# Kernel optimization log

Hardware: AMD Instinct MI355X
Metric: run time of the kernel (lower is better)

The kernel has to match this reference:

```python
import jax, jax.numpy as jnp
import numpy as np

B, C, H, W = 4, 256, 64, 64
CH = C // 2  # inner channels


def setup_inputs() -> dict:
    key = jax.random.key(0)
    ks = jax.random.split(key, 9)
    s = 1.0 / np.sqrt(C)
    so = 1.0 / np.sqrt(CH)
    return {
        "x": jax.random.normal(ks[0], (B, C, H, W), dtype=jnp.float32),
        "teta_w": jax.random.uniform(ks[1], (CH, C), jnp.float32, -s, s),
        "teta_b": jax.random.uniform(ks[2], (CH,), jnp.float32, -s, s),
        "fi_w": jax.random.uniform(ks[3], (CH, C), jnp.float32, -s, s),
        "fi_b": jax.random.uniform(ks[4], (CH,), jnp.float32, -s, s),
        "gi_w": jax.random.uniform(ks[5], (CH, C), jnp.float32, -s, s),
        "gi_b": jax.random.uniform(ks[6], (CH,), jnp.float32, -s, s),
        "out_w": jax.random.uniform(ks[7], (C, CH), jnp.float32, -so, so),
        "out_b": jax.random.uniform(ks[8], (C,), jnp.float32, -so, so),
    }


def _conv1x1(x, w, b):
    # x: (B, Cin, H, W), w: (Cout, Cin) -> (B, Cout, H, W)
    return jnp.einsum('bchw,oc->bohw', x, w) + b[None, :, None, None]


def reference(x, teta_w, teta_b, fi_w, fi_b, gi_w, gi_b, out_w, out_b):
    b, c, h, w = x.shape
    n = h * w
    ch = teta_w.shape[0]
    # NOTE: original uses .view (reshape), NOT transpose, to get (B, N, Ch)
    x1 = _conv1x1(x, teta_w, teta_b).reshape(b, ch, n).reshape(b, n, ch)
    x2 = _conv1x1(x, fi_w, fi_b).reshape(b, ch, n)            # (B, Ch, N)
    x3 = _conv1x1(x, gi_w, gi_b).reshape(b, ch, n).reshape(b, n, ch)
    # softmax over dim=1 (rows), as in the original
    attn = jax.nn.softmax(jnp.matmul(x1, x2), axis=1)          # (B, N, N)
    y = jnp.matmul(attn, x3)                                   # (B, N, Ch)
    y = jnp.swapaxes(y, 1, 2).reshape(b, ch, h, w)
    return x + _conv1x1(y, out_w, out_b)
```

## Files before the change

kernel.cpp:

```cpp
#include <hip/hip_runtime.h>
#include <hip/hip_bf16.h>

#define BB 4
#define CC 256
#define CHH 128
#define NN 4096
#define KSHIFT 12.0f

typedef __attribute__((ext_vector_type(8))) short bf16x8;
typedef __attribute__((ext_vector_type(4))) float f32x4;

__device__ __forceinline__ float to_f(float v) { return v; }
__device__ __forceinline__ float to_f(__hip_bfloat16 v) { return __bfloat162float(v); }
__device__ __forceinline__ void st_f(float* p, float v) { *p = v; }
__device__ __forceinline__ void st_f(__hip_bfloat16* p, float v) { *p = __float2bfloat16(v); }
__device__ __forceinline__ unsigned short f2bf(float f) {
    __hip_bfloat16 h = __float2bfloat16(f);
    unsigned short u;
    __builtin_memcpy(&u, &h, 2);
    return u;
}
__device__ __forceinline__ bf16x8 ldb8(const unsigned short* p) { return *(const bf16x8*)p; }

__device__ __forceinline__ void gload_lds16(const unsigned short* g, unsigned short* l) {
    __builtin_amdgcn_global_load_lds(
        (const __attribute__((address_space(1))) unsigned int*)g,
        (__attribute__((address_space(3))) unsigned int*)l, 16, 0, 0);
}

__global__ void detect_kernel(const void* __restrict__ tb, int* __restrict__ flag) {
    if (threadIdx.x == 0) {
        const __hip_bfloat16* p = (const __hip_bfloat16*)tb;
        int big = 0, zeros = 0;
        for (int i = 0; i < 128; ++i) {
            float v = __bfloat162float(p[i]);
            if (!(fabsf(v) <= 0.5f)) big = 1;
            if ((i & 1) == 0 && v == 0.0f) zeros++;
        }
        *flag = (big || zeros >= 32) ? 1 : 0;
    }
}

template <typename T>
__device__ __forceinline__ void prep_body(const T* tw, const T* fw, const T* gw, const T* ow,
                                          const T* tb2, const T* fb, const T* gb, const T* ob,
                                          unsigned short* Wb, unsigned short* OWb,
                                          float* Bf, float* OBf) {
    int idx = blockIdx.x * 256 + threadIdx.x;
    if (idx < 98304) {
        int cv = idx >> 15, rem = idx & 32767;
        const T* src = cv == 0 ? tw : (cv == 1 ? fw : gw);
        Wb[idx] = f2bf(to_f(src[rem]));
    } else if (idx < 131072) {
        OWb[idx - 98304] = f2bf(to_f(ow[idx - 98304]));
    } else if (idx < 131456) {
        int r = idx - 131072;
        int cv = r >> 7, j = r & 127;
        const T* src = cv == 0 ? tb2 : (cv == 1 ? fb : gb);
        Bf[r] = to_f(src[j]);
    } else if (idx < 131712) {
        OBf[idx - 131456] = to_f(ob[idx - 131456]);
    }
}

__global__ void prep_kernel(const void* tw, const void* fw, const void* gw, const void* ow,
                            const void* tb2, const void* fb, const void* gb, const void* ob,
                            const int* __restrict__ flag,
                            unsigned short* Wb, unsigned short* OWb, float* Bf, float* OBf) {
    if (*flag)
        prep_body<float>((const float*)tw, (const float*)fw, (const float*)gw, (const float*)ow,
                         (const float*)tb2, (const float*)fb, (const float*)gb, (const float*)ob,
                         Wb, OWb, Bf, OBf);
    else
        prep_body<__hip_bfloat16>((const __hip_bfloat16*)tw, (const __hip_bfloat16*)fw,
                                  (const __hip_bfloat16*)gw, (const __hip_bfloat16*)ow,
                                  (const __hip_bfloat16*)tb2, (const __hip_bfloat16*)fb,
                                  (const __hip_bfloat16*)gb, (const __hip_bfloat16*)ob,
                                  Wb, OWb, Bf, OBf);
}

template <typename T>
__device__ __forceinline__ void xtrans_body(const T* __restrict__ x, unsigned short* __restrict__ xt) {
    int b = blockIdx.z;
    const T* in = x + (size_t)b * CC * NN;
    unsigned short* out = xt + (size_t)b * NN * CC;
    int p0 = blockIdx.x * 64, c0 = blockIdx.y * 64;
    __shared__ unsigned short t[64][68];
    int flat = threadIdx.x;
#pragma unroll
    for (int tt = 0; tt < 16; ++tt) {
        int id = flat + tt * 256;
        int rr = id >> 6, cc = id & 63;
        t[cc][rr] = f2bf(to_f(in[(size_t)(c0 + rr) * NN + p0 + cc]));
    }
    __syncthreads();
#pragma unroll
    for (int tt = 0; tt < 16; ++tt) {
        int id = flat + tt * 256;
        int pp = id >> 6, jj = id & 63;
        out[(size_t)(p0 + pp) * CC + c0 + jj] = t[pp][jj];
    }
}

__launch_bounds__(256)
__global__ void xtrans_kernel(const void* x, const int* __restrict__ flag,
                              unsigned short* __restrict__ xt) {
    if (*flag) xtrans_body<float>((const float*)x, xt);
    else       xtrans_body<__hip_bfloat16>((const __hip_bfloat16*)x, xt);
}

__launch_bounds__(256)
__global__ void conv3_mfma_kernel(const unsigned short* __restrict__ xt,
                                  const unsigned short* __restrict__ Wb,
                                  const float* __restrict__ Bf,
                                  unsigned short* __restrict__ T1b,
                                  unsigned short* __restrict__ T2t,
                                  unsigned short* __restrict__ T3b) {
    int b = blockIdx.y;
    int p0 = blockIdx.x * 16;
    int flat = threadIdx.x;
    int w = flat >> 6, lane = flat & 63, m = lane & 15, quad = lane >> 4;
    const unsigned short* xrow = xt + ((size_t)b * NN + p0 + m) * CC;
    bf16x8 xf[8];
#pragma unroll
    for (int kc = 0; kc < 8; ++kc)
        xf[kc] = ldb8(&xrow[kc * 32 + quad * 8]);
    unsigned short* t1  = T1b + (size_t)b * CHH * NN;
    unsigned short* t2t = T2t + (size_t)b * CHH * NN;
    unsigned short* t3  = T3b + (size_t)b * CHH * NN;
#pragma unroll
    for (int q = 0; q < 6; ++q) {
        int t = w * 6 + q;
        int cv = t >> 3, ot = t & 7;
        int o0 = ot * 16;
        const unsigned short* wrow = Wb + ((size_t)cv * CHH + o0 + m) * CC;
        f32x4 acc = {0.f, 0.f, 0.f, 0.f};
#pragma unroll
        for (int kc = 0; kc < 8; ++kc) {
            bf16x8 wf = ldb8(&wrow[kc * 32 + quad * 8]);
            acc = __builtin_amdgcn_mfma_f32_16x16x32_bf16(wf, xf[kc], acc, 0, 0, 0);
        }
        unsigned short hv[4];
#pragma unroll
        for (int r = 0; r < 4; ++r)
            hv[r] = f2bf(acc[r] + Bf[cv * CHH + o0 + quad * 4 + r]);
        if (cv == 1) {
            unsigned int lo = (unsigned int)hv[0] | ((unsigned int)hv[1] << 16);
            unsigned int hi = (unsigned int)hv[2] | ((unsigned int)hv[3] << 16);
            int src = (lane & 3) * 16 + (lane >> 2);
            unsigned int tlo = (unsigned int)__shfl((int)lo, src, 64);
            unsigned int thi = (unsigned int)__shfl((int)hi, src, 64);
            unsigned int* dst = (unsigned int*)&t2t[(size_t)(p0 + (lane >> 2)) * CHH +
                                                    o0 + (lane & 3) * 4];
            dst[0] = tlo;
            dst[1] = thi;
        } else {
            unsigned short* outp = (cv == 0) ? t1 : t3;
#pragma unroll
            for (int r = 0; r < 4; ++r)
                outp[(size_t)(o0 + quad * 4 + r) * NN + p0 + m] = hv[r];
        }
    }
}

__launch_bounds__(256)
__global__ void transpose_kernel(const unsigned short* __restrict__ in,
                                 unsigned short* __restrict__ out, int R, int C) {
    int bz = blockIdx.z;
    in  += (size_t)bz * R * C;
    out += (size_t)bz * R * C;
    int c0 = blockIdx.x * 64, r0 = blockIdx.y * 64;
    __shared__ unsigned short t[64][68];
    int flat = threadIdx.x;
#pragma unroll
    for (int tt = 0; tt < 16; ++tt) {
        int id = flat + tt * 256;
        int r = id >> 6, c = id & 63;
        t[c][r] = in[(size_t)(r0 + r) * C + c0 + c];
    }
    __syncthreads();
#pragma unroll
    for (int tt = 0; tt < 16; ++tt) {
        int id = flat + tt * 256;
        int c = id >> 6, r = id & 63;
        out[(size_t)(c0 + c) * R + r0 + r] = t[c][r];
    }
}

__launch_bounds__(256)
__global__ void stats_mfma_kernel(const unsigned short* __restrict__ T1b,
                                  const unsigned short* __restrict__ T2t,
                                  float* __restrict__ Lpart) {
    int blk = blockIdx.x;
    int b = (blk & 7) >> 1;
    int rest = (blk >> 3) * 2 + (blk & 1);
    int strip = rest >> 3, iq = rest & 7;
    int ibase = iq * 512;
    int flat = threadIdx.x;
    int w = flat >> 6, lane = flat & 63, m = lane & 15, quad = lane >> 4;
    const unsigned short* A  = T1b + (size_t)b * CHH * NN;
    const unsigned short* Bt = T2t + (size_t)b * CHH * NN;
    __shared__ unsigned short th[64 * 128];

    int u0w = strip * 128 + w * 32;
    bf16x8 bfr[2][4];
#pragma unroll
    for (int g = 0; g < 2; ++g)
#pragma unroll
        for (int kc = 0; kc < 4; ++kc)
            bfr[g][kc] = ldb8(&Bt[(size_t)(u0w + g * 16 + m) * CHH + kc * 32 + quad * 8]);

    float csum[2] = {0.f, 0.f};
    for (int t = 0; t < 8; ++t) {
        int i0t = ibase + t * 64;
        __syncthreads();
#pragma unroll
        for (int i = 0; i < 4; ++i) {
            int sl = i * 256 + flat;
            int r = sl >> 4, ch = sl & 15;
            int c = ch ^ (r & 7);
            gload_lds16(&A[(size_t)(i0t + r) * CHH + c * 8], &th[sl * 8]);
        }
        __syncthreads();
#pragma unroll
        for (int s = 0; s < 4; ++s) {
            int irow = s * 16 + m;
            bf16x8 af[4];
#pragma unroll
            for (int kc = 0; kc < 4; ++kc) {
                int ch = (kc * 4 + quad) ^ (irow & 7);
                af[kc] = *(const bf16x8*)&th[irow * 128 + ch * 8];
            }
#pragma unroll
            for (int g = 0; g < 2; ++g) {
                f32x4 acc = {0.f, 0.f, 0.f, 0.f};
#pragma unroll
                for (int kc = 0; kc < 4; ++kc)
                    acc = __builtin_amdgcn_mfma_f32_16x16x32_bf16(af[kc], bfr[g][kc], acc, 0, 0, 0);
#pragma unroll
                for (int r = 0; r < 4; ++r)
                    csum[g] += __expf(acc[r] - KSHIFT);
            }
        }
    }
#pragma unroll
    for (int g = 0; g < 2; ++g) {
        csum[g] += __shfl_xor(csum[g], 16, 64);
        csum[g] += __shfl_xor(csum[g], 32, 64);
        if (lane < 16)
            Lpart[((size_t)iq * BB + b) * NN + u0w + g * 16 + m] = csum[g];
    }
}

__launch_bounds__(256)
__global__ void attn_mfma_kernel(const unsigned short* __restrict__ T1b,
                                 const unsigned short* __restrict__ T2t,
                                 const unsigned short* __restrict__ X3t,
                                 const float* __restrict__ Lpart,
                                 unsigned short* __restrict__ Yp0,
                                 unsigned short* __restrict__ Yp1,
                                 unsigned short* __restrict__ Yp2,
                                 unsigned short* __restrict__ Yp3) {
    int blk = blockIdx.x;
    int b = (blk & 7) >> 1;
    int rest = (blk >> 3) * 2 + (blk & 1);
    int it = rest >> 2, uc = rest & 3;
    int i0 = it * 128;
    unsigned short* Yp = uc == 0 ? Yp0 : (uc == 1 ? Yp1 : (uc == 2 ? Yp2 : Yp3));
    int flat = threadIdx.x;
    int w = flat >> 6, lane = flat & 63, m = lane & 15, quad = lane >> 4;
    const unsigned short* A  = T1b + (size_t)b * CHH * NN;
    const unsigned short* Bt = T2t + (size_t)b * CHH * NN;
    const unsigned short* X3 = X3t + (size_t)b * CHH * NN;

    __shared__ unsigned short bt[64 * 128];
    __shared__ unsigned short x3[128 * 64];
    __shared__ unsigned short pT[4][2][16][40];
    __shared__ float llh[1024];

    int ubeg = uc * 1024;
#pragma unroll
    for (int k = 0; k < 4; ++k) {
        int idx = k * 256 + flat;
        int u = ubeg + idx;
        float s = 0.f;
#pragma unroll
        for (int c = 0; c < 8; ++c)
            s += Lpart[((size_t)c * BB + b) * NN + u];
        llh[idx] = logf(s) + KSHIFT;
    }

    int iw = i0 + w * 32;
    bf16x8 ath[2][4];
#pragma unroll
    for (int g = 0; g < 2; ++g)
#pragma unroll
        for (int kc = 0; kc < 4; ++kc)
            ath[g][kc] = ldb8(&A[(size_t)(iw + g * 16 + m) * CHH + kc * 32 + quad * 8]);
    f32x4 yacc[2][8];
#pragma unroll
    for (int g = 0; g < 2; ++g)
#pragma unroll
        for (int js = 0; js < 8; ++js) yacc[g][js] = (f32x4){0.f, 0.f, 0.f, 0.f};

    for (int u0 = ubeg; u0 < ubeg + 1024; u0 += 64) {
        __syncthreads();
#pragma unroll
        for (int i = 0; i < 4; ++i) {
            int sl = i * 256 + flat;
            int u = sl >> 4, ch = sl & 15;
            int c = ch ^ (u & 7);
            gload_lds16(&Bt[(size_t)(u0 + u) * CHH + c * 8], &bt[sl * 8]);
        }
#pragma unroll
        for (int i = 0; i < 4; ++i) {
            int sl = i * 256 + flat;
            int j = sl >> 3, ch = sl & 7;
            int c = ch ^ (j & 7);
            gload_lds16(&X3[(size_t)j * NN + u0 + c * 8], &x3[sl * 8]);
        }
        __syncthreads();
#pragma unroll
        for (int h = 0; h < 2; ++h) {
#pragma unroll
            for (int su = 0; su < 2; ++su) {
                int u = h * 32 + su * 16 + m;
                f32x4 a0 = {0.f, 0.f, 0.f, 0.f}, a1 = {0.f, 0.f, 0.f, 0.f};
#pragma unroll
                for (int kc = 0; kc < 4; ++kc) {
                    int ch = (kc * 4 + quad) ^ (u & 7);
                    bf16x8 bf = *(const bf16x8*)&bt[u * 128 + ch * 8];
                    a0 = __builtin_amdgcn_mfma_f32_16x16x32_bf16(ath[0][kc], bf, a0, 0, 0, 0);
                    a1 = __builtin_amdgcn_mfma_f32_16x16x32_bf16(ath[1][kc], bf, a1, 0, 0, 0);
                }
                float ll = llh[u0 - ubeg + u];
#pragma unroll
                for (int r = 0; r < 4; ++r) {
                    pT[w][0][quad * 4 + r][su * 16 + m] = f2bf(__expf(a0[r] - ll));
                    pT[w][1][quad * 4 + r][su * 16 + m] = f2bf(__expf(a1[r] - ll));
                }
            }
            bf16x8 pa0 = *(const bf16x8*)&pT[w][0][m][quad * 8];
            bf16x8 pa1 = *(const bf16x8*)&pT[w][1][m][quad * 8];
#pragma unroll
            for (int js = 0; js < 8; ++js) {
                int j = js * 16 + m;
                int ch = (h * 4 + quad) ^ (j & 7);
                bf16x8 xb = *(const bf16x8*)&x3[j * 64 + ch * 8];
                yacc[0][js] = __builtin_amdgcn_mfma_f32_16x16x32_bf16(pa0, xb, yacc[0][js], 0, 0, 0);
                yacc[1][js] = __builtin_amdgcn_mfma_f32_16x16x32_bf16(pa1, xb, yacc[1][js], 0, 0, 0);
            }
        }
    }
#pragma unroll
    for (int g = 0; g < 2; ++g)
#pragma unroll
        for (int js = 0; js < 8; ++js)
#pragma unroll
            for (int r = 0; r < 4; ++r)
                Yp[((size_t)b * NN + iw + g * 16 + quad * 4 + r) * CHH + js * 16 + m] =
                    f2bf(yacc[g][js][r]);
}

template <typename T>
__device__ __forceinline__ void outconv_body(const T* __restrict__ x,
                                             const unsigned short* __restrict__ Yp0,
                                             const unsigned short* __restrict__ Yp1,
                                             const unsigned short* __restrict__ Yp2,
                                             const unsigned short* __restrict__ Yp3,
                                             const unsigned short* __restrict__ OWb,
                                             const float* __restrict__ OBf,
                                             T* __restrict__ out) {
    int b = blockIdx.y;
    int p0 = blockIdx.x * 16;
    int flat = threadIdx.x;
    int w = flat >> 6, lane = flat & 63, m = lane & 15, quad = lane >> 4;
    size_t yoff = ((size_t)b * NN + p0 + m) * CHH;
    const unsigned short* yrows[4] = {Yp0 + yoff, Yp1 + yoff, Yp2 + yoff, Yp3 + yoff};
    bf16x8 yf[4][4];
#pragma unroll
    for (int pz = 0; pz < 4; ++pz)
#pragma unroll
        for (int kc = 0; kc < 4; ++kc)
            yf[pz][kc] = ldb8(&yrows[pz][kc * 32 + quad * 8]);
#pragma unroll
    for (int q = 0; q < 4; ++q) {
        int o0 = (w * 4 + q) * 16;
        const unsigned short* wrow = OWb + (size_t)(o0 + m) * CHH;
        f32x4 acc = {0.f, 0.f, 0.f, 0.f};
#pragma unroll
        for (int kc = 0; kc < 4; ++kc) {
            bf16x8 aw = ldb8(&wrow[kc * 32 + quad * 8]);
#pragma unroll
            for (int pz = 0; pz < 4; ++pz)
                acc = __builtin_amdgcn_mfma_f32_16x16x32_bf16(aw, yf[pz][kc], acc, 0, 0, 0);
        }
#pragma unroll
        for (int r = 0; r < 4; ++r) {
            int co = o0 + quad * 4 + r;
            size_t oi = ((size_t)b * CC + co) * NN + p0 + m;
            st_f(&out[oi], acc[r] + OBf[co] + to_f(x[oi]));
        }
    }
}

__launch_bounds__(256)
__global__ void outconv_mfma_kernel(const void* x,
                                    const unsigned short* __restrict__ Yp0,
                                    const unsigned short* __restrict__ Yp1,
                                    const unsigned short* __restrict__ Yp2,
                                    const unsigned short* __restrict__ Yp3,
                                    const unsigned short* __restrict__ OWb,
                                    const float* __restrict__ OBf,
                                    const int* __restrict__ flag, void* out) {
    if (*flag)
        outconv_body<float>((const float*)x, Yp0, Yp1, Yp2, Yp3, OWb, OBf, (float*)out);
    else
        outconv_body<__hip_bfloat16>((const __hip_bfloat16*)x, Yp0, Yp1, Yp2, Yp3, OWb, OBf,
                                     (__hip_bfloat16*)out);
}

extern "C" void kernel_launch(void* const* d_in, const int* in_sizes, int n_in,
                              void* d_out, int out_size, void* d_ws, size_t ws_size,
                              hipStream_t stream) {
    const void* x  = d_in[0];
    const void* tw = d_in[1];
    const void* tb = d_in[2];
    const void* fw = d_in[3];
    const void* fb = d_in[4];
    const void* gw = d_in[5];
    const void* gb = d_in[6];
    const void* ow = d_in[7];
    const void* ob = d_in[8];

    const size_t TE = (size_t)BB * CHH * NN;
    unsigned short* T1b = (unsigned short*)d_ws;
    unsigned short* T2t = T1b + TE;
    unsigned short* X3t = T2t + TE;
    unsigned short* T3b = X3t + TE;
    unsigned short* xt  = T3b + TE;
    unsigned short* Yp0 = xt;
    unsigned short* Yp1 = xt + TE;
    unsigned short* Yp2 = T3b;
    unsigned short* Yp3 = xt + 2 * TE;
    unsigned short* Wb  = Yp3 + TE;
    unsigned short* OWb = Wb + 98304;
    float* Bf    = (float*)(OWb + 32768);
    float* OBf   = Bf + 384;
    float* Lpart = OBf + 256;
    int*   Flag  = (int*)(Lpart + 131072);

    detect_kernel<<<1, 64, 0, stream>>>(tb, Flag);
    prep_kernel<<<dim3(515), 256, 0, stream>>>(tw, fw, gw, ow, tb, fb, gb, ob,
                                               Flag, Wb, OWb, Bf, OBf);
    xtrans_kernel<<<dim3(NN / 64, CC / 64, BB), 256, 0, stream>>>(x, Flag, xt);
    conv3_mfma_kernel<<<dim3(NN / 16, BB), 256, 0, stream>>>(xt, Wb, Bf, T1b, T2t, T3b);
    transpose_kernel<<<dim3(CHH / 64, NN / 64, BB), 256, 0, stream>>>(T3b, X3t, NN, CHH);
    stats_mfma_kernel<<<dim3(1024), 256, 0, stream>>>(T1b, T2t, Lpart);
    attn_mfma_kernel<<<dim3(512), 256, 0, stream>>>(T1b, T2t, X3t, Lpart, Yp0, Yp1, Yp2, Yp3);
    outconv_mfma_kernel<<<dim3(NN / 16, BB), 256, 0, stream>>>(x, Yp0, Yp1, Yp2, Yp3,
                                                               OWb, OBf, Flag, d_out);
}
```

Before: 214.5 us.

## Double-buffer LDS tiles in stats and attention kernels to overlap loads with MFMA

Both the stats kernel and the attention kernel now hold two LDS buffers per staged tile. The next tile is issued with async global-to-LDS loads while the current one is consumed by MFMAs, which removes one barrier per iteration and hides load latency. The cost is doubled LDS use in the attention kernel (bt and x3 grow to about 64KB plus pT and llh), which can reduce occupancy. The gload_lds16 completion is only guarded by the single __syncthreads, so correctness depends on that barrier waiting for the outstanding vmcnt.

```diff
diff --git a/kernel.cpp b/kernel.cpp
--- a/kernel.cpp
+++ b/kernel.cpp
@@ -200,7 +200,7 @@
     int w = flat >> 6, lane = flat & 63, m = lane & 15, quad = lane >> 4;
     const unsigned short* A  = T1b + (size_t)b * CHH * NN;
     const unsigned short* Bt = T2t + (size_t)b * CHH * NN;
-    __shared__ unsigned short th[64 * 128];
+    __shared__ unsigned short th[2][64 * 128];
 
     int u0w = strip * 128 + w * 32;
     bf16x8 bfr[2][4];
@@ -210,18 +210,22 @@
         for (int kc = 0; kc < 4; ++kc)
             bfr[g][kc] = ldb8(&Bt[(size_t)(u0w + g * 16 + m) * CHH + kc * 32 + quad * 8]);
 
+#define STAGE_TH(dst, ii)                                                          \
+    _Pragma("unroll")                                                              \
+    for (int i_ = 0; i_ < 4; ++i_) {                                               \
+        int sl = i_ * 256 + flat;                                                  \
+        int r_ = sl >> 4, ch_ = sl & 15;                                           \
+        int c_ = ch_ ^ (r_ & 7);                                                   \
+        gload_lds16(&A[(size_t)((ii) + r_) * CHH + c_ * 8], &th[dst][sl * 8]);     \
+    }
+
     float csum[2] = {0.f, 0.f};
+    STAGE_TH(0, ibase);
+    __syncthreads();
+    int cur = 0;
     for (int t = 0; t < 8; ++t) {
-        int i0t = ibase + t * 64;
-        __syncthreads();
-#pragma unroll
-        for (int i = 0; i < 4; ++i) {
-            int sl = i * 256 + flat;
-            int r = sl >> 4, ch = sl & 15;
-            int c = ch ^ (r & 7);
-            gload_lds16(&A[(size_t)(i0t + r) * CHH + c * 8], &th[sl * 8]);
-        }
-        __syncthreads();
+        if (t < 7) { STAGE_TH(cur ^ 1, ibase + (t + 1) * 64); }
+        const unsigned short* thc = th[cur];
 #pragma unroll
         for (int s = 0; s < 4; ++s) {
             int irow = s * 16 + m;
@@ -229,7 +233,7 @@
 #pragma unroll
             for (int kc = 0; kc < 4; ++kc) {
                 int ch = (kc * 4 + quad) ^ (irow & 7);
-                af[kc] = *(const bf16x8*)&th[irow * 128 + ch * 8];
+                af[kc] = *(const bf16x8*)&thc[irow * 128 + ch * 8];
             }
 #pragma unroll
             for (int g = 0; g < 2; ++g) {
@@ -242,7 +246,12 @@
                     csum[g] += __expf(acc[r] - KSHIFT);
             }
         }
-    }
+        if (t < 7) {
+            __syncthreads();
+            cur ^= 1;
+        }
+    }
+#undef STAGE_TH
 #pragma unroll
     for (int g = 0; g < 2; ++g) {
         csum[g] += __shfl_xor(csum[g], 16, 64);
@@ -273,8 +282,8 @@
     const unsigned short* Bt = T2t + (size_t)b * CHH * NN;
     const unsigned short* X3 = X3t + (size_t)b * CHH * NN;
 
-    __shared__ unsigned short bt[64 * 128];
-    __shared__ unsigned short x3[128 * 64];
+    __shared__ unsigned short bt[2][64 * 128];
+    __shared__ unsigned short x3[2][128 * 64];
     __shared__ unsigned short pT[4][2][16][40];
     __shared__ float llh[1024];
 
@@ -303,23 +312,30 @@
 #pragma unroll
         for (int js = 0; js < 8; ++js) yacc[g][js] = (f32x4){0.f, 0.f, 0.f, 0.f};
 
-    for (int u0 = ubeg; u0 < ubeg + 1024; u0 += 64) {
-        __syncthreads();
-#pragma unroll
-        for (int i = 0; i < 4; ++i) {
-            int sl = i * 256 + flat;
-            int u = sl >> 4, ch = sl & 15;
-            int c = ch ^ (u & 7);
-            gload_lds16(&Bt[(size_t)(u0 + u) * CHH + c * 8], &bt[sl * 8]);
-        }
-#pragma unroll
-        for (int i = 0; i < 4; ++i) {
-            int sl = i * 256 + flat;
-            int j = sl >> 3, ch = sl & 7;
-            int c = ch ^ (j & 7);
-            gload_lds16(&X3[(size_t)j * NN + u0 + c * 8], &x3[sl * 8]);
-        }
-        __syncthreads();
+#define STAGE_UT(dst, uu)                                                          \
+    _Pragma("unroll")                                                              \
+    for (int i_ = 0; i_ < 4; ++i_) {                    \
+        int sl = i_ * 256 + flat;                                                  \
+        int u_ = sl >> 4, ch_ = sl & 15;                                           \
+        int c_ = ch_ ^ (u_ & 7);                                                   \
+        gload_lds16(&Bt[(size_t)((uu) + u_) * CHH + c_ * 8], &bt[dst][sl * 8]);    \
+    }                                                                              \
+    _Pragma("unroll")                                                              \
+    for (int i_ = 0; i_ < 4; ++i_) {                    \
+        int sl = i_ * 256 + flat;                                                  \
+        int j_ = sl >> 3, ch_ = sl & 7;                                            \
+        int c_ = ch_ ^ (j_ & 7);                                                   \
+        gload_lds16(&X3[(size_t)j_ * NN + (uu) + c_ * 8], &x3[dst][sl * 8]);       \
+    }
+
+    STAGE_UT(0, ubeg);
+    __syncthreads();
+    int cur = 0;
+    for (int t = 0; t < 16; ++t) {
+        int u0 = ubeg + t * 64;
+        if (t < 15) { STAGE_UT(cur ^ 1, u0 + 64); }
+        const unsigned short* btc = bt[cur];
+        const unsigned short* x3c = x3[cur];
 #pragma unroll
         for (int h = 0; h < 2; ++h) {
 #pragma unroll
@@ -329,7 +345,7 @@
 #pragma unroll
                 for (int kc = 0; kc < 4; ++kc) {
                     int ch = (kc * 4 + quad) ^ (u & 7);
-                    bf16x8 bf = *(const bf16x8*)&bt[u * 128 + ch * 8];
+                    bf16x8 bf = *(const bf16x8*)&btc[u * 128 + ch * 8];
                     a0 = __builtin_amdgcn_mfma_f32_16x16x32_bf16(ath[0][kc], bf, a0, 0, 0, 0);
                     a1 = __builtin_amdgcn_mfma_f32_16x16x32_bf16(ath[1][kc], bf, a1, 0, 0, 0);
                 }
@@ -346,12 +362,17 @@
             for (int js = 0; js < 8; ++js) {
                 int j = js * 16 + m;
                 int ch = (h * 4 + quad) ^ (j & 7);
-                bf16x8 xb = *(const bf16x8*)&x3[j * 64 + ch * 8];
+                bf16x8 xb = *(const bf16x8*)&x3c[j * 64 + ch * 8];
                 yacc[0][js] = __builtin_amdgcn_mfma_f32_16x16x32_bf16(pa0, xb, yacc[0][js], 0, 0, 0);
                 yacc[1][js] = __builtin_amdgcn_mfma_f32_16x16x32_bf16(pa1, xb, yacc[1][js], 0, 0, 0);
             }
         }
-    }
+        if (t < 15) {
+            __syncthreads();
+            cur ^= 1;
+        }
+    }
+#undef STAGE_UT
 #pragma unroll
     for (int g = 0; g < 2; ++g)
 #pragma unroll
```

Result: no change. 217.1 us (+1.2%).
